# Optimization experiments

Measured on AMD Instinct MI355X. Metric: run time of the kernel, lower is better.

## Reference

```python
import jax, jax.numpy as jnp
import numpy as np

D = 2          # qudit dimension
L = 22         # number of qudits; state length = D**L = 4194304
INDEX = tuple(range(L))  # rotation applied on every qudit (angle[i] indexed by qudit position)

# Generator S = Sx(j=0, k=1) on a D-level system: |0><1| + |1><0|
def _make_S():
    S = np.zeros((D, D), dtype=np.complex64)
    S[0, 1] = 1.0
    S[1, 0] = 1.0
    return jnp.asarray(S)


def setup_inputs() -> dict:
    key = jax.random.key(0)
    k1, k2, k3 = jax.random.split(key, 3)
    n = D ** L
    x_real = jax.random.normal(k1, (n,), dtype=jnp.float32)
    x_imag = jax.random.normal(k2, (n,), dtype=jnp.float32)
    angle = jax.random.uniform(k3, (L,), dtype=jnp.float32)
    return {"x_real": x_real, "x_imag": x_imag, "angle": angle}


def reference(x_real, x_imag, angle):
    # U = kron_i expm(-0.5j * angle[i] * S)  (identity on qudits not in INDEX),
    # applied as U @ x. Instead of materializing the D^L x D^L sparse unitary,
    # apply each single-qudit gate by contracting axis i of the reshaped state,
    # which is exactly the same linear map.
    S = _make_S()
    psi = (x_real + 1j * x_imag).astype(jnp.complex64).reshape((D,) * L)
    for i in range(L):
        if i in INDEX:
            M = jax.scipy.linalg.expm((-0.5j) * angle[i].astype(jnp.complex64) * S)
            # contract qudit axis i: psi'[..., a, ...] = sum_b M[a,b] psi[..., b, ...]
            psi = jnp.moveaxis(jnp.tensordot(M, psi, axes=([1], [i])), 0, i)
        # else: identity, nothing to do
    out = psi.reshape(-1)
    return jnp.stack([out.real, out.imag])  # (2, D**L) float32
```

## Files before the change

kernel.cpp:

```cpp
#include <hip/hip_runtime.h>


constexpr int NTOT = 1 << 22;

__device__ __forceinline__ void rotg(float& ar, float& ai, float& br, float& bi,
                                     float c, float s) {
    float t0 = ar, t1 = ai, t2 = br, t3 = bi;
    ar = fmaf(c, t0,  s * t3);
    ai = fmaf(c, t1, -s * t2);
    br = fmaf(c, t2,  s * t1);
    bi = fmaf(c, t3, -s * t0);
}

__device__ __forceinline__ void build_cs(const float* __restrict__ ang,
                                         float* cs_c, float* cs_s, int t) {
    if (t < 22) {
        float a = 0.5f * ang[21 - t];
        cs_c[t] = cosf(a);
        cs_s[t] = sinf(a);
    }
}

__device__ __forceinline__ int padslot(int i) { return i + (i >> 4) + (i >> 8); }

__global__ __launch_bounds__(256, 4) void rgate_low(const float* __restrict__ xr,
                                                    const float* __restrict__ xi,
                                                    const float* __restrict__ ang,
                                                    float* __restrict__ out) {
    __shared__ float2 sv[4368];
    __shared__ float cs_c[22], cs_s[22];
    const int t  = threadIdx.x;
    const int g0 = blockIdx.x << 12;

    build_cs(ang, cs_c, cs_s, t);

    float ar[16], ai[16];
    const float* xrp = xr + g0 + t;
    const float* xip = xi + g0 + t;
    #pragma unroll
    for (int j = 0; j < 16; ++j) {
        ar[j] = xrp[j << 8];
        ai[j] = xip[j << 8];
    }
    __syncthreads();

    #pragma unroll
    for (int b = 0; b < 4; ++b) {
        const int m = 1 << b;
        const float c = cs_c[8 + b], s = cs_s[8 + b];
        #pragma unroll
        for (int j = 0; j < 16; ++j)
            if (!(j & m)) rotg(ar[j], ai[j], ar[j | m], ai[j | m], c, s);
    }
    #pragma unroll
    for (int j = 0; j < 16; ++j)
        sv[padslot(t + (j << 8))] = make_float2(ar[j], ai[j]);
    __syncthreads();

    {
        const int base2 = (t & 15) + ((t >> 4) << 8);
        #pragma unroll
        for (int j = 0; j < 16; ++j) {
            float2 v = sv[padslot(base2 + (j << 4))];
            ar[j] = v.x; ai[j] = v.y;
        }
        #pragma unroll
        for (int b = 0; b < 4; ++b) {
            const int m = 1 << b;
            const float c = cs_c[4 + b], s = cs_s[4 + b];
            #pragma unroll
            for (int j = 0; j < 16; ++j)
                if (!(j & m)) rotg(ar[j], ai[j], ar[j | m], ai[j | m], c, s);
        }
        #pragma unroll
        for (int j = 0; j < 16; ++j)
            sv[padslot(base2 + (j << 4))] = make_float2(ar[j], ai[j]);
    }
    __syncthreads();

    {
        const int base3 = t << 4;
        #pragma unroll
        for (int j = 0; j < 16; ++j) {
            float2 v = sv[padslot(base3 + j)];
            ar[j] = v.x; ai[j] = v.y;
        }
        #pragma unroll
        for (int b = 0; b < 4; ++b) {
            const int m = 1 << b;
            const float c = cs_c[b], s = cs_s[b];
            #pragma unroll
            for (int j = 0; j < 16; ++j)
                if (!(j & m)) rotg(ar[j], ai[j], ar[j | m], ai[j | m], c, s);
        }
        float4* orp = (float4*)(out + g0 + base3);
        float4* oip = (float4*)(out + NTOT + g0 + base3);
        #pragma unroll
        for (int q = 0; q < 4; ++q) {
            orp[q] = make_float4(ar[4*q], ar[4*q+1], ar[4*q+2], ar[4*q+3]);
            oip[q] = make_float4(ai[4*q], ai[4*q+1], ai[4*q+2], ai[4*q+3]);
        }
    }
}

__global__ __launch_bounds__(256) void rgate_mid(const float* __restrict__ ang,
                                                 float* __restrict__ out) {
    __shared__ float2 sv[2048];
    __shared__ float cs_c[22], cs_s[22];
    const int t    = threadIdx.x;
    const int lane = t & 63, w = t >> 6;
    const int bid  = blockIdx.x;
    const int base = ((bid >> 6) << 17) + ((bid & 63) << 6) + lane;
    float* outr = out;
    float* outi = out + NTOT;

    build_cs(ang, cs_c, cs_s, t);

    float ar[8], ai[8];
    #pragma unroll
    for (int j = 0; j < 8; ++j) {
        const int g = base + ((j | (w << 3)) << 12);
        ar[j] = outr[g]; ai[j] = outi[g];
    }
    __syncthreads();

    #pragma unroll
    for (int b = 0; b < 3; ++b) {
        const int m = 1 << b;
        const float c = cs_c[12 + b], s = cs_s[12 + b];
        #pragma unroll
        for (int j = 0; j < 8; ++j)
            if (!(j & m)) rotg(ar[j], ai[j], ar[j | m], ai[j | m], c, s);
    }
    #pragma unroll
    for (int j = 0; j < 8; ++j)
        sv[((j | (w << 3)) << 6) + lane] = make_float2(ar[j], ai[j]);
    __syncthreads();

    #pragma unroll
    for (int j = 0; j < 8; ++j) {
        const int h = ((j & 3) << 3) | (w << 1) | (j >> 2);
        float2 v = sv[(h << 6) + lane];
        ar[j] = v.x; ai[j] = v.y;
    }
    #pragma unroll
    for (int b = 0; b < 2; ++b) {
        const int m = 1 << b;
        const float c = cs_c[15 + b], s = cs_s[15 + b];
        #pragma unroll
        for (int j = 0; j < 8; ++j)
            if (!(j & m)) rotg(ar[j], ai[j], ar[j | m], ai[j | m], c, s);
    }
    #pragma unroll
    for (int j = 0; j < 8; ++j) {
        const int h = ((j & 3) << 3) | (w << 1) | (j >> 2);
        const int g = base + (h << 12);
        outr[g] = ar[j]; outi[g] = ai[j];
    }
}

__global__ __launch_bounds__(256) void rgate_high(const float* __restrict__ ang,
                                                  float* __restrict__ out) {
    __shared__ float2 sv[2048];
    __shared__ float cs_c[22], cs_s[22];
    const int t    = threadIdx.x;
    const int lane = t & 63, w = t >> 6;
    const int base = (blockIdx.x << 6) + lane;
    float* outr = out;
    float* outi = out + NTOT;

    build_cs(ang, cs_c, cs_s, t);

    float ar[8], ai[8];
    #pragma unroll
    for (int j = 0; j < 8; ++j) {
        const int g = ((j | (w << 3)) << 17) + base;
        ar[j] = outr[g]; ai[j] = outi[g];
    }
    __syncthreads();

    #pragma unroll
    for (int b = 0; b < 3; ++b) {
        const int m = 1 << b;
        const float c = cs_c[17 + b], s = cs_s[17 + b];
        #pragma unroll
        for (int j = 0; j < 8; ++j)
            if (!(j & m)) rotg(ar[j], ai[j], ar[j | m], ai[j | m], c, s);
    }
    #pragma unroll
    for (int j = 0; j < 8; ++j)
        sv[((j | (w << 3)) << 6) + lane] = make_float2(ar[j], ai[j]);
    __syncthreads();

    #pragma unroll
    for (int j = 0; j < 8; ++j) {
        const int u = ((j & 3) << 3) | (w << 1) | (j >> 2);
        float2 v = sv[(u << 6) + lane];
        ar[j] = v.x; ai[j] = v.y;
    }
    #pragma unroll
    for (int b = 0; b < 2; ++b) {
        const int m = 1 << b;
        const float c = cs_c[20 + b], s = cs_s[20 + b];
        #pragma unroll
        for (int j = 0; j < 8; ++j)
            if (!(j & m)) rotg(ar[j], ai[j], ar[j | m], ai[j | m], c, s);
    }
    #pragma unroll
    for (int j = 0; j < 8; ++j) {
        const int u = ((j & 3) << 3) | (w << 1) | (j >> 2);
        const int g = (u << 17) + base;
        outr[g] = ar[j]; outi[g] = ai[j];
    }
}

extern "C" void kernel_launch(void* const* d_in, const int* in_sizes, int n_in,
                              void* d_out, int out_size, void* d_ws, size_t ws_size,
                              hipStream_t stream) {
    const float* xr  = (const float*)d_in[0];
    const float* xi  = (const float*)d_in[1];
    const float* ang = (const float*)d_in[2];
    float* out = (float*)d_out;

    rgate_low<<<1024, 256, 0, stream>>>(xr, xi, ang, out);
    rgate_mid<<<2048, 256, 0, stream>>>(ang, out);
    rgate_high<<<2048, 256, 0, stream>>>(ang, out);
}
```

Measured before the change: 112.3 us.

## Merge three gate passes into two with 16K-element shared-memory tiles

The first kernel now applies 14 qubit rotations inside one 16384-element tile using 1024-thread blocks and an XOR-swizzled shared layout. A second kernel handles the remaining 8 high qubits. This removes one full read/write sweep of the 32 MB state, cutting HBM traffic by about a third. Sin/cos are now computed per thread instead of once into shared memory. The trade-offs are 128 KB of shared memory per block, which limits occupancy, and only 256 blocks per launch on a 256-CU device.

```diff
diff --git a/kernel.cpp b/kernel.cpp
--- a/kernel.cpp
+++ b/kernel.cpp
@@ -12,204 +12,114 @@
     bi = fmaf(c, t3, -s * t0);
 }
 
-__device__ __forceinline__ void build_cs(const float* __restrict__ ang,
-                                         float* cs_c, float* cs_s, int t) {
-    if (t < 22) {
-        float a = 0.5f * ang[21 - t];
-        cs_c[t] = cosf(a);
-        cs_s[t] = sinf(a);
-    }
-}
-
-__device__ __forceinline__ int padslot(int i) { return i + (i >> 4) + (i >> 8); }
-
-__global__ __launch_bounds__(256, 4) void rgate_low(const float* __restrict__ xr,
-                                                    const float* __restrict__ xi,
-                                                    const float* __restrict__ ang,
-                                                    float* __restrict__ out) {
-    __shared__ float2 sv[4368];
-    __shared__ float cs_c[22], cs_s[22];
-    const int t  = threadIdx.x;
-    const int g0 = blockIdx.x << 12;
-
-    build_cs(ang, cs_c, cs_s, t);
-
-    float ar[16], ai[16];
-    const float* xrp = xr + g0 + t;
-    const float* xip = xi + g0 + t;
+template<int K0, int NB>
+__device__ __forceinline__ void gates(float (&ar)[16], float (&ai)[16],
+                                      const float* __restrict__ ang) {
     #pragma unroll
-    for (int j = 0; j < 16; ++j) {
-        ar[j] = xrp[j << 8];
-        ai[j] = xip[j << 8];
-    }
-    __syncthreads();
-
-    #pragma unroll
-    for (int b = 0; b < 4; ++b) {
+    for (int b = 0; b < NB; ++b) {
         const int m = 1 << b;
-        const float c = cs_c[8 + b], s = cs_s[8 + b];
+        const float a = 0.5f * ang[21 - (K0 + b)];
+        const float c = cosf(a), s = sinf(a);
         #pragma unroll
         for (int j = 0; j < 16; ++j)
             if (!(j & m)) rotg(ar[j], ai[j], ar[j | m], ai[j | m], c, s);
     }
+}
+
+__device__ __forceinline__ int slotA(int i) { return i ^ ((i >> 4) & 15); }
+
+__global__ __launch_bounds__(1024) void rgate_low14(const float* __restrict__ xr,
+                                                    const float* __restrict__ xi,
+                                                    const float* __restrict__ ang,
+                                                    float* __restrict__ out) {
+    __shared__ float2 sv[16384];
+    const int t  = threadIdx.x;
+    const int g0 = blockIdx.x << 14;
+
+    float ar[16], ai[16];
+    #pragma unroll
+    for (int j = 0; j < 16; ++j) {
+        ar[j] = xr[g0 + t + (j << 10)];
+        ai[j] = xi[g0 + t + (j << 10)];
+    }
+
+    gates<10, 4>(ar, ai, ang);
     #pragma unroll
     for (int j = 0; j < 16; ++j)
-        sv[padslot(t + (j << 8))] = make_float2(ar[j], ai[j]);
+        sv[slotA(t + (j << 10))] = make_float2(ar[j], ai[j]);
     __syncthreads();
 
-    {
-        const int base2 = (t & 15) + ((t >> 4) << 8);
-        #pragma unroll
-        for (int j = 0; j < 16; ++j) {
-            float2 v = sv[padslot(base2 + (j << 4))];
-            ar[j] = v.x; ai[j] = v.y;
-        }
-        #pragma unroll
-        for (int b = 0; b < 4; ++b) {
-            const int m = 1 << b;
-            const float c = cs_c[4 + b], s = cs_s[4 + b];
-            #pragma unroll
-            for (int j = 0; j < 16; ++j)
-                if (!(j & m)) rotg(ar[j], ai[j], ar[j | m], ai[j | m], c, s);
-        }
-        #pragma unroll
-        for (int j = 0; j < 16; ++j)
-            sv[padslot(base2 + (j << 4))] = make_float2(ar[j], ai[j]);
+    const int base2 = (t & 63) + ((t >> 6) << 10);
+    #pragma unroll
+    for (int j = 0; j < 16; ++j) {
+        float2 v = sv[slotA(base2 + (j << 6))];
+        ar[j] = v.x; ai[j] = v.y;
     }
+    gates<6, 4>(ar, ai, ang);
+    #pragma unroll
+    for (int j = 0; j < 16; ++j)
+        sv[slotA(base2 + (j << 6))] = make_float2(ar[j], ai[j]);
     __syncthreads();
 
-    {
-        const int base3 = t << 4;
-        #pragma unroll
-        for (int j = 0; j < 16; ++j) {
-            float2 v = sv[padslot(base3 + j)];
-            ar[j] = v.x; ai[j] = v.y;
-        }
-        #pragma unroll
-        for (int b = 0; b < 4; ++b) {
-            const int m = 1 << b;
-            const float c = cs_c[b], s = cs_s[b];
-            #pragma unroll
-            for (int j = 0; j < 16; ++j)
-                if (!(j & m)) rotg(ar[j], ai[j], ar[j | m], ai[j | m], c, s);
-        }
-        float4* orp = (float4*)(out + g0 + base3);
-        float4* oip = (float4*)(out + NTOT + g0 + base3);
-        #pragma unroll
-        for (int q = 0; q < 4; ++q) {
-            orp[q] = make_float4(ar[4*q], ar[4*q+1], ar[4*q+2], ar[4*q+3]);
-            oip[q] = make_float4(ai[4*q], ai[4*q+1], ai[4*q+2], ai[4*q+3]);
-        }
+    const int base3 = (t & 3) + ((t >> 2) << 6);
+    #pragma unroll
+    for (int j = 0; j < 16; ++j) {
+        float2 v = sv[slotA(base3 + (j << 2))];
+        ar[j] = v.x; ai[j] = v.y;
+    }
+    gates<2, 4>(ar, ai, ang);
+    #pragma unroll
+    for (int j = 0; j < 16; ++j)
+        sv[slotA(base3 + (j << 2))] = make_float2(ar[j], ai[j]);
+    __syncthreads();
+
+    const int base4 = t << 4;
+    #pragma unroll
+    for (int j = 0; j < 16; ++j) {
+        float2 v = sv[slotA(base4 + j)];
+        ar[j] = v.x; ai[j] = v.y;
+    }
+    gates<0, 2>(ar, ai, ang);
+    float4* orp = (float4*)(out + g0 + base4);
+    float4* oip = (float4*)(out + NTOT + g0 + base4);
+    #pragma unroll
+    for (int q = 0; q < 4; ++q) {
+        orp[q] = make_float4(ar[4*q], ar[4*q+1], ar[4*q+2], ar[4*q+3]);
+        oip[q] = make_float4(ai[4*q], ai[4*q+1], ai[4*q+2], ai[4*q+3]);
     }
 }
 
-__global__ __launch_bounds__(256) void rgate_mid(const float* __restrict__ ang,
-                                                 float* __restrict__ out) {
-    __shared__ float2 sv[2048];
-    __shared__ float cs_c[22], cs_s[22];
-    const int t    = threadIdx.x;
-    const int lane = t & 63, w = t >> 6;
-    const int bid  = blockIdx.x;
-    const int base = ((bid >> 6) << 17) + ((bid & 63) << 6) + lane;
-    float* outr = out;
-    float* outi = out + NTOT;
-
-    build_cs(ang, cs_c, cs_s, t);
-
-    float ar[8], ai[8];
-    #pragma unroll
-    for (int j = 0; j < 8; ++j) {
-        const int g = base + ((j | (w << 3)) << 12);
-        ar[j] = outr[g]; ai[j] = outi[g];
-    }
-    __syncthreads();
-
-    #pragma unroll
-    for (int b = 0; b < 3; ++b) {
-        const int m = 1 << b;
-        const float c = cs_c[12 + b], s = cs_s[12 + b];
-        #pragma unroll
-        for (int j = 0; j < 8; ++j)
-            if (!(j & m)) rotg(ar[j], ai[j], ar[j | m], ai[j | m], c, s);
-    }
-    #pragma unroll
-    for (int j = 0; j < 8; ++j)
-        sv[((j | (w << 3)) << 6) + lane] = make_float2(ar[j], ai[j]);
-    __syncthreads();
-
-    #pragma unroll
-    for (int j = 0; j < 8; ++j) {
-        const int h = ((j & 3) << 3) | (w << 1) | (j >> 2);
-        float2 v = sv[(h << 6) + lane];
-        ar[j] = v.x; ai[j] = v.y;
-    }
-    #pragma unroll
-    for (int b = 0; b < 2; ++b) {
-        const int m = 1 << b;
-        const float c = cs_c[15 + b], s = cs_s[15 + b];
-        #pragma unroll
-        for (int j = 0; j < 8; ++j)
-            if (!(j & m)) rotg(ar[j], ai[j], ar[j | m], ai[j | m], c, s);
-    }
-    #pragma unroll
-    for (int j = 0; j < 8; ++j) {
-        const int h = ((j & 3) << 3) | (w << 1) | (j >> 2);
-        const int g = base + (h << 12);
-        outr[g] = ar[j]; outi[g] = ai[j];
-    }
-}
-
-__global__ __launch_bounds__(256) void rgate_high(const float* __restrict__ ang,
-                                                  float* __restrict__ out) {
-    __shared__ float2 sv[2048];
-    __shared__ float cs_c[22], cs_s[22];
+__global__ __launch_bounds__(1024) void rgate_high8(const float* __restrict__ ang,
+                                                    float* __restrict__ out) {
+    __shared__ float2 sv[16384];
     const int t    = threadIdx.x;
     const int lane = t & 63, w = t >> 6;
     const int base = (blockIdx.x << 6) + lane;
     float* outr = out;
     float* outi = out + NTOT;
 
-    build_cs(ang, cs_c, cs_s, t);
-
-    float ar[8], ai[8];
+    float ar[16], ai[16];
     #pragma unroll
-    for (int j = 0; j < 8; ++j) {
-        const int g = ((j | (w << 3)) << 17) + base;
+    for (int j = 0; j < 16; ++j) {
+        const int g = ((j | (w << 4)) << 14) + base;
         ar[j] = outr[g]; ai[j] = outi[g];
     }
+
+    gates<14, 4>(ar, ai, ang);
+    #pragma unroll
+    for (int j = 0; j < 16; ++j)
+        sv[((j | (w << 4)) << 6) + lane] = make_float2(ar[j], ai[j]);
     __syncthreads();
 
     #pragma unroll
-    for (int b = 0; b < 3; ++b) {
-        const int m = 1 << b;
-        const float c = cs_c[17 + b], s = cs_s[17 + b];
-        #pragma unroll
-        for (int j = 0; j < 8; ++j)
-            if (!(j & m)) rotg(ar[j], ai[j], ar[j | m], ai[j | m], c, s);
-    }
-    #pragma unroll
-    for (int j = 0; j < 8; ++j)
-        sv[((j | (w << 3)) << 6) + lane] = make_float2(ar[j], ai[j]);
-    __syncthreads();
-
-    #pragma unroll
-    for (int j = 0; j < 8; ++j) {
-        const int u = ((j & 3) << 3) | (w << 1) | (j >> 2);
-        float2 v = sv[(u << 6) + lane];
+    for (int j = 0; j < 16; ++j) {
+        float2 v = sv[((w | (j << 4)) << 6) + lane];
         ar[j] = v.x; ai[j] = v.y;
     }
+    gates<18, 4>(ar, ai, ang);
     #pragma unroll
-    for (int b = 0; b < 2; ++b) {
-        const int m = 1 << b;
-        const float c = cs_c[20 + b], s = cs_s[20 + b];
-        #pragma unroll
-        for (int j = 0; j < 8; ++j)
-            if (!(j & m)) rotg(ar[j], ai[j], ar[j | m], ai[j | m], c, s);
-    }
-    #pragma unroll
-    for (int j = 0; j < 8; ++j) {
-        const int u = ((j & 3) << 3) | (w << 1) | (j >> 2);
-        const int g = (u << 17) + base;
+    for (int j = 0; j < 16; ++j) {
+        const int g = ((w | (j << 4)) << 14) + base;
         outr[g] = ar[j]; outi[g] = ai[j];
     }
 }
@@ -222,7 +132,6 @@
     const float* ang = (const float*)d_in[2];
     float* out = (float*)d_out;
 
-    rgate_low<<<1024, 256, 0, stream>>>(xr, xi, ang, out);
-    rgate_mid<<<2048, 256, 0, stream>>>(ang, out);
-    rgate_high<<<2048, 256, 0, stream>>>(ang, out);
+    rgate_low14<<<256, 1024, 0, stream>>>(xr, xi, ang, out);
+    rgate_high8<<<256, 1024, 0, stream>>>(ang, out);
 }
```

Measured after the change: 116.0 us. +3.2%, slower.
